# Performance work log

Measured on AMD Instinct MI355X. Metric: run time of the kernel, lower is better.

The kernel has to match this reference:

```python
import jax, jax.numpy as jnp
import numpy as np

B = 8192          # batch
FEAT = 14 * 14 * (16 + 4)  # 3920 features per image
NUM_CLASSES = 10
REPS = 8          # CX+RY repetitions in the filter circuit


def _filter_probs(p):
    """Analytic output distribution of the 4-qubit filter circuit.
    p: (..., 4) pixel angles [p0, p1, p2, p3].
    Circuit: RY(p_i) on qubit i, then 8x [CX(0,1); RY(p0,0)], measure all.
    Qubits 2,3 stay in product state; evolve (q0,q1) as a real 2x2 amplitude
    grid a[q0, q1]. Output index = q0*8 + q1*4 + q2*2 + q3 (Qiskit bitstring
    reversed as in the torch source).
    """
    h = 0.5 * p
    c, s = jnp.cos(h), jnp.sin(h)
    v0 = jnp.stack([c[..., 0], s[..., 0]], axis=-1)
    v1 = jnp.stack([c[..., 1], s[..., 1]], axis=-1)
    a = v0[..., :, None] * v1[..., None, :]        # (..., 2, 2) amplitudes a[q0,q1]
    c0, s0 = c[..., 0], s[..., 0]
    R0 = jnp.stack([jnp.stack([c0, -s0], axis=-1),
                    jnp.stack([s0,  c0], axis=-1)], axis=-2)  # RY(p0) matrix
    for _ in range(REPS):
        # CX(control=q0, target=q1): flip q1 where q0 == 1
        a = jnp.stack([a[..., 0, :], a[..., 1, ::-1]], axis=-2)
        # RY(p0) on q0
        a = jnp.einsum('...ik,...kj->...ij', R0, a)
    P01 = a * a                                    # joint probs over (q0, q1)
    p2 = s[..., 2] ** 2                            # P(q2 = 1)
    p3 = s[..., 3] ** 2                            # P(q3 = 1)
    P2 = jnp.stack([1.0 - p2, p2], axis=-1)
    P3 = jnp.stack([1.0 - p3, p3], axis=-1)
    P = (P01[..., :, :, None, None]
         * P2[..., None, None, :, None]
         * P3[..., None, None, None, :])           # (..., q0, q1, q2, q3)
    return P.reshape(P.shape[:-4] + (16,))


def _sampler_probs(tl, br):
    """2-qubit sampler with all weights = 0: the two CX(0,1) cancel, so the
    state is RY(tl)|0> x RY(br)|0>. Output index = q0*2 + q1."""
    s0 = jnp.sin(0.5 * tl) ** 2   # P(q0 = 1)
    s1 = jnp.sin(0.5 * br) ** 2   # P(q1 = 1)
    return jnp.stack([(1 - s0) * (1 - s1), (1 - s0) * s1,
                      s0 * (1 - s1), s0 * s1], axis=-1)


def setup_inputs() -> dict:
    key = jax.random.key(0)
    k1, k2 = jax.random.split(key)
    x = jax.random.uniform(k1, (B, 1, 28, 28), dtype=jnp.float32)
    fc_w = jax.random.normal(k2, (NUM_CLASSES, FEAT), dtype=jnp.float32) * (FEAT ** -0.5)
    fc_b = jnp.zeros((NUM_CLASSES,), dtype=jnp.float32)
    return {"x": x, "fc_w": fc_w, "fc_b": fc_b}


def reference(x, fc_w, fc_b):
    b = x.shape[0]
    # (b, 14, 14, 2, 2) patches; patch[u, v] = img[2i+u, 2j+v]
    patches = x.reshape(b, 14, 2, 14, 2).transpose(0, 1, 3, 2, 4)
    p = patches.reshape(b, 196, 4)                 # [p0, p1, p2, p3] per patch
    filter_feats = _filter_probs(p).reshape(b, -1)            # (b, 196*16)
    sampler_feats = _sampler_probs(patches[..., 0, 0],
                                   patches[..., 1, 1]).reshape(b, -1)  # (b, 196*4)
    feats = jnp.concatenate([filter_feats, sampler_feats], axis=-1)
    logits = feats @ fc_w.T + fc_b
    return jax.nn.log_softmax(logits, axis=-1)
```

## Files before the change

### kernel.cpp

```cpp
#include <hip/hip_runtime.h>
#include <hip/hip_bf16.h>

typedef float v2f __attribute__((ext_vector_type(2)));
typedef short short8 __attribute__((ext_vector_type(8)));
typedef float f32x4 __attribute__((ext_vector_type(4)));

#define NCLS  10
#define FEATN 3920
#define GIMG  16
#define RSTR  996

__device__ __forceinline__ unsigned packbf(float a, float b) {
    __hip_bfloat162 h = __float22bfloat162_rn(float2{a, b});
    unsigned u; __builtin_memcpy(&u, &h, 4); return u;
}

__global__ void conv_w(const float* __restrict__ fc_w, __hip_bfloat16* __restrict__ ws) {
    const int id = blockIdx.x * 256 + threadIdx.x;
    const int kb = id >> 9;
    const int r  = id & 511;
    const int l  = r >> 3;
    const int j  = r & 7;
    const int n  = l & 15;
    const int k  = kb * 32 + ((l >> 4) << 3) + j;
    const float w = (n < NCLS && k < FEATN) ? fc_w[n * FEATN + k] : 0.f;
    ws[id] = __float2bfloat16(w);
}

__device__ __forceinline__ void do_filter(const float* __restrict__ base, int p, int q,
                                          int dw, unsigned* __restrict__ lds) {
    const int pi = p / 14, pj = p - pi * 14;
    const int offT = pi * 56 + pj * 2;
    const float* iA = base + (size_t)(2 * q) * 784;
    const float* iB = iA + 784;
    const float2 tA = *reinterpret_cast<const float2*>(iA + offT);
    const float2 bA = *reinterpret_cast<const float2*>(iA + offT + 28);
    const float2 tB = *reinterpret_cast<const float2*>(iB + offT);
    const float2 bB = *reinterpret_cast<const float2*>(iB + offT + 28);

    float sA0,cA0,sA1,cA1,sA2,cA2,sA3,cA3;
    float sB0,cB0,sB1,cB1,sB2,cB2,sB3,cB3;
    __sincosf(0.5f * tA.x, &sA0, &cA0); __sincosf(0.5f * tA.y, &sA1, &cA1);
    __sincosf(0.5f * bA.x, &sA2, &cA2); __sincosf(0.5f * bA.y, &sA3, &cA3);
    __sincosf(0.5f * tB.x, &sB0, &cB0); __sincosf(0.5f * tB.y, &sB1, &cB1);
    __sincosf(0.5f * bB.x, &sB2, &cB2); __sincosf(0.5f * bB.y, &sB3, &cB3);

    const v2f c0 = {cA0, cB0}, s0 = {sA0, sB0};
    const v2f c1 = {cA1, cB1}, s1 = {sA1, sB1};
    v2f a00 = c0 * c1, a01 = c0 * s1, a10 = s0 * c1, a11 = s0 * s1;
    #pragma unroll
    for (int r = 0; r < 8; ++r) {
        const v2f b10 = a11, b11 = a10;
        const v2f n00 = c0 * a00 - s0 * b10;
        const v2f n01 = c0 * a01 - s0 * b11;
        const v2f n10 = s0 * a00 + c0 * b10;
        const v2f n11 = s0 * a01 + c0 * b11;
        a00 = n00; a01 = n01; a10 = n10; a11 = n11;
    }
    v2f P2[4];
    P2[0] = a00 * a00; P2[1] = a01 * a01; P2[2] = a10 * a10; P2[3] = a11 * a11;
    const v2f t2c = {cA2*cA2, cB2*cB2}, t2s = {sA2*sA2, sB2*sB2};
    const v2f t3c = {cA3*cA3, cB3*cB3}, t3s = {sA3*sA3, sB3*sB3};
    v2f T[4];
    T[0] = t2c * t3c; T[1] = t2c * t3s; T[2] = t2s * t3c; T[3] = t2s * t3s;

    unsigned dA[8], dB[8];
    #pragma unroll
    for (int m = 0; m < 4; ++m) {
        const v2f f0 = P2[m] * T[0], f1 = P2[m] * T[1];
        const v2f f2 = P2[m] * T[2], f3 = P2[m] * T[3];
        dA[2*m]   = packbf(f0.x, f1.x); dA[2*m+1] = packbf(f2.x, f3.x);
        dB[2*m]   = packbf(f0.y, f1.y); dB[2*m+1] = packbf(f2.y, f3.y);
    }
    unsigned* rowA = lds + (2 * q) * RSTR + dw;
    unsigned* rowB = rowA + RSTR;
    *reinterpret_cast<uint4*>(rowA)     = uint4{dA[0], dA[1], dA[2], dA[3]};
    *reinterpret_cast<uint4*>(rowA + 4) = uint4{dA[4], dA[5], dA[6], dA[7]};
    *reinterpret_cast<uint4*>(rowB)     = uint4{dB[0], dB[1], dB[2], dB[3]};
    *reinterpret_cast<uint4*>(rowB + 4) = uint4{dB[4], dB[5], dB[6], dB[7]};
}

__device__ __forceinline__ void do_sampler(const float* __restrict__ base, int p, int q,
                                           unsigned* __restrict__ lds) {
    const int pi = p / 14, pj = p - pi * 14;
    const int offT = pi * 56 + pj * 2;
    const float* iA = base + (size_t)(2 * q) * 784;
    const float* iB = iA + 784;
    const float p0A = iA[offT],  p3A = iA[offT + 29];
    const float p0B = iB[offT],  p3B = iB[offT + 29];
    const float sA = __sinf(0.5f * p0A), tA = __sinf(0.5f * p3A);
    const float sB = __sinf(0.5f * p0B), tB = __sinf(0.5f * p3B);
    const float saA = sA*sA, sbA = tA*tA, naA = 1.f - saA, nbA = 1.f - sbA;
    const float saB = sB*sB, sbB = tB*tB, naB = 1.f - saB, nbB = 1.f - sbB;
    const int dw = 576 + 2 * p;
    *reinterpret_cast<uint2*>(lds + (2*q)   * RSTR + dw) =
        uint2{packbf(naA*nbA, naA*sbA), packbf(saA*nbA, saA*sbA)};
    *reinterpret_cast<uint2*>(lds + (2*q+1) * RSTR + dw) =
        uint2{packbf(naB*nbB, naB*sbB), packbf(saB*nbB, saB*sbB)};
}

__global__ __launch_bounds__(256, 2)
void quanv_mfma(const float* __restrict__ x,
                const short* __restrict__ wsb,
                const float* __restrict__ fc_b,
                float* __restrict__ out) {
    __shared__ __align__(16) unsigned lds[GIMG * RSTR];
    const int tid  = threadIdx.x;
    const int img0 = blockIdx.x * GIMG;
    const float* base = x + (size_t)img0 * 784;
    const int lane = tid & 63;
    const int wave = tid >> 6;
    const int am   = lane & 15;
    const int ach  = lane >> 4;
    const unsigned aoff = am * RSTR + ach * 4;

    f32x4 acc = {0.f, 0.f, 0.f, 0.f};

    #pragma unroll
    for (int i = 0; i < 4; ++i) {
        const int tau = tid + (i << 8);
        if (tau < 992) do_filter(base, tau >> 3, tau & 7, (tau >> 3) << 3, lds);
    }
    __syncthreads();
    for (int kb = wave; kb < 62; kb += 4) {
        const short8 a = *reinterpret_cast<const short8*>(lds + aoff + kb * 16);
        const short8 b = *reinterpret_cast<const short8*>(wsb + (size_t)kb * 512 + lane * 8);
        acc = __builtin_amdgcn_mfma_f32_16x16x32_bf16(a, b, acc, 0, 0, 0);
    }
    __syncthreads();

    #pragma unroll
    for (int i = 0; i < 3; ++i) {
        const int tau = tid + (i << 8);
        if (tau < 576) {
            const int p = 124 + (tau >> 3);
            do_filter(base, p, tau & 7, (p - 124) << 3, lds);
        }
    }
    #pragma unroll
    for (int i = 0; i < 7; ++i) {
        const int ka = tid + (i << 8);
        if (ka < 1568) do_sampler(base, ka >> 3, ka & 7, lds);
    }
    if (tid < GIMG) {
        unsigned* z = lds + tid * RSTR + 968;
        *reinterpret_cast<uint4*>(z)     = uint4{0, 0, 0, 0};
        *reinterpret_cast<uint4*>(z + 4) = uint4{0, 0, 0, 0};
    }
    __syncthreads();
    for (int kb = wave; kb < 61; kb += 4) {
        const short8 a = *reinterpret_cast<const short8*>(lds + aoff + kb * 16);
        const short8 b = *reinterpret_cast<const short8*>(wsb + (size_t)(62 + kb) * 512 + lane * 8);
        acc = __builtin_amdgcn_mfma_f32_16x16x32_bf16(a, b, acc, 0, 0, 0);
    }
    __syncthreads();

    float* f = reinterpret_cast<float*>(lds);
    f[wave * 256 +   0 + lane] = acc[0];
    f[wave * 256 +  64 + lane] = acc[1];
    f[wave * 256 + 128 + lane] = acc[2];
    f[wave * 256 + 192 + lane] = acc[3];
    __syncthreads();
    if (tid < GIMG * NCLS) {
        const int g = tid / NCLS, c = tid - g * NCLS;
        const int li = ((g >> 2) << 4) + c;
        const int ri = (g & 3) << 6;
        float v = f[ri + li] + f[256 + ri + li] + f[512 + ri + li] + f[768 + ri + li];
        f[1024 + tid] = v + fc_b[c];
    }
    __syncthreads();
    if (tid < GIMG * NCLS) {
        const int g = tid / NCLS, c = tid - g * NCLS;
        const float* lg = f + 1024 + g * NCLS;
        float m = -1e30f;
        #pragma unroll
        for (int k = 0; k < NCLS; ++k) m = fmaxf(m, lg[k]);
        float ss = 0.f;
        #pragma unroll
        for (int k = 0; k < NCLS; ++k) ss += __expf(lg[k] - m);
        out[(size_t)(img0 + g) * NCLS + c] = lg[c] - m - __logf(ss);
    }
}

extern "C" void kernel_launch(void* const* d_in, const int* in_sizes, int n_in,
                              void* d_out, int out_size, void* d_ws, size_t ws_size,
                              hipStream_t stream) {
    const float* x    = (const float*)d_in[0];
    const float* fc_w = (const float*)d_in[1];
    const float* fc_b = (const float*)d_in[2];
    float* out = (float*)d_out;

    conv_w<<<246, 256, 0, stream>>>(fc_w, (__hip_bfloat16*)d_ws);

    const int B = in_sizes[0] / 784;
    const int grid = B / GIMG;
    quanv_mfma<<<grid, 256, 0, stream>>>(x, (const short*)d_ws, fc_b, out);
}
```

Measured before the change: 88.34 us.

## Fuse sampler into filter pass, chunk patches into four stages, halve images per block

Reorders the weight matrix so that each chunk of 48 (or 52) patches has its filter and sampler features contiguous. Each thread computes sampler probabilities from the sincos values it already has, so the separate sampler pass and its extra global loads go away. All pixels are preloaded into registers up front, and the GEMM runs in four chunked stages with a smaller LDS buffer. Images per block drop from 16 to 8 to raise occupancy. Half of the MFMA M dimension now holds duplicate rows, and each stage adds extra barriers.

```diff
diff --git a/kernel.cpp b/kernel.cpp
--- a/kernel.cpp
+++ b/kernel.cpp
@@ -7,8 +7,8 @@
 
 #define NCLS  10
 #define FEATN 3920
-#define GIMG  16
-#define RSTR  996
+#define GIMG  8
+#define RSTR  532
 
 __device__ __forceinline__ unsigned packbf(float a, float b) {
     __hip_bfloat162 h = __float22bfloat162_rn(float2{a, b});
@@ -17,143 +17,138 @@
 
 __global__ void conv_w(const float* __restrict__ fc_w, __hip_bfloat16* __restrict__ ws) {
     const int id = blockIdx.x * 256 + threadIdx.x;
-    const int kb = id >> 9;
-    const int r  = id & 511;
-    const int l  = r >> 3;
-    const int j  = r & 7;
+    if (id >= 123 * 512) return;
+    const int kb = id >> 9, r = id & 511, l = r >> 3, j0 = r & 7;
     const int n  = l & 15;
-    const int k  = kb * 32 + ((l >> 4) << 3) + j;
-    const float w = (n < NCLS && k < FEATN) ? fc_w[n * FEATN + k] : 0.f;
+    const int kk = kb * 32 + ((l >> 4) << 3) + j0;
+    float w = 0.f;
+    if (n < NCLS) {
+        const int t    = (kk < 2880) ? kk / 960 : 3;
+        const int base = 960 * t;
+        const int P0   = 48 * t;
+        const int np   = (t == 3) ? 52 : 48;
+        const int u    = kk - base;
+        int korig = -1;
+        if (u < np * 16) {
+            korig = 16 * (P0 + (u >> 4)) + (u & 15);
+        } else {
+            const int v = u - np * 16;
+            if (v < np * 4) korig = 3136 + 4 * (P0 + (v >> 2)) + (v & 3);
+        }
+        if (korig >= 0) w = fc_w[n * FEATN + korig];
+    }
     ws[id] = __float2bfloat16(w);
 }
 
-__device__ __forceinline__ void do_filter(const float* __restrict__ base, int p, int q,
-                                          int dw, unsigned* __restrict__ lds) {
-    const int pi = p / 14, pj = p - pi * 14;
-    const int offT = pi * 56 + pj * 2;
-    const float* iA = base + (size_t)(2 * q) * 784;
-    const float* iB = iA + 784;
-    const float2 tA = *reinterpret_cast<const float2*>(iA + offT);
-    const float2 bA = *reinterpret_cast<const float2*>(iA + offT + 28);
-    const float2 tB = *reinterpret_cast<const float2*>(iB + offT);
-    const float2 bB = *reinterpret_cast<const float2*>(iB + offT + 28);
-
-    float sA0,cA0,sA1,cA1,sA2,cA2,sA3,cA3;
-    float sB0,cB0,sB1,cB1,sB2,cB2,sB3,cB3;
-    __sincosf(0.5f * tA.x, &sA0, &cA0); __sincosf(0.5f * tA.y, &sA1, &cA1);
-    __sincosf(0.5f * bA.x, &sA2, &cA2); __sincosf(0.5f * bA.y, &sA3, &cA3);
-    __sincosf(0.5f * tB.x, &sB0, &cB0); __sincosf(0.5f * tB.y, &sB1, &cB1);
-    __sincosf(0.5f * bB.x, &sB2, &cB2); __sincosf(0.5f * bB.y, &sB3, &cB3);
-
-    const v2f c0 = {cA0, cB0}, s0 = {sA0, sB0};
-    const v2f c1 = {cA1, cB1}, s1 = {sA1, sB1};
-    v2f a00 = c0 * c1, a01 = c0 * s1, a10 = s0 * c1, a11 = s0 * s1;
-    #pragma unroll
-    for (int r = 0; r < 8; ++r) {
-        const v2f b10 = a11, b11 = a10;
-        const v2f n00 = c0 * a00 - s0 * b10;
-        const v2f n01 = c0 * a01 - s0 * b11;
-        const v2f n10 = s0 * a00 + c0 * b10;
-        const v2f n11 = s0 * a01 + c0 * b11;
-        a00 = n00; a01 = n01; a10 = n10; a11 = n11;
-    }
-    v2f P2[4];
-    P2[0] = a00 * a00; P2[1] = a01 * a01; P2[2] = a10 * a10; P2[3] = a11 * a11;
-    const v2f t2c = {cA2*cA2, cB2*cB2}, t2s = {sA2*sA2, sB2*sB2};
-    const v2f t3c = {cA3*cA3, cB3*cB3}, t3s = {sA3*sA3, sB3*sB3};
-    v2f T[4];
-    T[0] = t2c * t3c; T[1] = t2c * t3s; T[2] = t2s * t3c; T[3] = t2s * t3s;
-
-    unsigned dA[8], dB[8];
-    #pragma unroll
-    for (int m = 0; m < 4; ++m) {
-        const v2f f0 = P2[m] * T[0], f1 = P2[m] * T[1];
-        const v2f f2 = P2[m] * T[2], f3 = P2[m] * T[3];
-        dA[2*m]   = packbf(f0.x, f1.x); dA[2*m+1] = packbf(f2.x, f3.x);
-        dB[2*m]   = packbf(f0.y, f1.y); dB[2*m+1] = packbf(f2.y, f3.y);
-    }
-    unsigned* rowA = lds + (2 * q) * RSTR + dw;
-    unsigned* rowB = rowA + RSTR;
-    *reinterpret_cast<uint4*>(rowA)     = uint4{dA[0], dA[1], dA[2], dA[3]};
-    *reinterpret_cast<uint4*>(rowA + 4) = uint4{dA[4], dA[5], dA[6], dA[7]};
-    *reinterpret_cast<uint4*>(rowB)     = uint4{dB[0], dB[1], dB[2], dB[3]};
-    *reinterpret_cast<uint4*>(rowB + 4) = uint4{dB[4], dB[5], dB[6], dB[7]};
-}
-
-__device__ __forceinline__ void do_sampler(const float* __restrict__ base, int p, int q,
-                                           unsigned* __restrict__ lds) {
-    const int pi = p / 14, pj = p - pi * 14;
-    const int offT = pi * 56 + pj * 2;
-    const float* iA = base + (size_t)(2 * q) * 784;
-    const float* iB = iA + 784;
-    const float p0A = iA[offT],  p3A = iA[offT + 29];
-    const float p0B = iB[offT],  p3B = iB[offT + 29];
-    const float sA = __sinf(0.5f * p0A), tA = __sinf(0.5f * p3A);
-    const float sB = __sinf(0.5f * p0B), tB = __sinf(0.5f * p3B);
-    const float saA = sA*sA, sbA = tA*tA, naA = 1.f - saA, nbA = 1.f - sbA;
-    const float saB = sB*sB, sbB = tB*tB, naB = 1.f - saB, nbB = 1.f - sbB;
-    const int dw = 576 + 2 * p;
-    *reinterpret_cast<uint2*>(lds + (2*q)   * RSTR + dw) =
-        uint2{packbf(naA*nbA, naA*sbA), packbf(saA*nbA, saA*sbA)};
-    *reinterpret_cast<uint2*>(lds + (2*q+1) * RSTR + dw) =
-        uint2{packbf(naB*nbB, naB*sbB), packbf(saB*nbB, saB*sbB)};
-}
-
-__global__ __launch_bounds__(256, 2)
+__global__ __launch_bounds__(256, 4)
 void quanv_mfma(const float* __restrict__ x,
                 const short* __restrict__ wsb,
                 const float* __restrict__ fc_b,
                 float* __restrict__ out) {
     __shared__ __align__(16) unsigned lds[GIMG * RSTR];
     const int tid  = threadIdx.x;
+    const int lane = tid & 63;
+    const int wave = tid >> 6;
     const int img0 = blockIdx.x * GIMG;
     const float* base = x + (size_t)img0 * 784;
-    const int lane = tid & 63;
-    const int wave = tid >> 6;
-    const int am   = lane & 15;
-    const int ach  = lane >> 4;
-    const unsigned aoff = am * RSTR + ach * 4;
+    const int am  = lane & 15;
+    const int ach = lane >> 4;
+    const unsigned aoff = (unsigned)((am & 7) * RSTR + ach * 4);
+
+    float2 pix[4][4];
+    int lpv[4], qv[4];
+    bool act[4];
+    #pragma unroll
+    for (int t = 0; t < 4; ++t) {
+        const int np = (t == 3) ? 52 : 48;
+        const int P0 = 48 * t;
+        const bool a = tid < np * 4;
+        const int tt = a ? tid : 0;
+        const int q  = tt / np;
+        const int lp = tt - q * np;
+        const int p  = P0 + lp;
+        const int pi = p / 14, pj = p - pi * 14;
+        const int off = pi * 56 + pj * 2;
+        const float* iA = base + (size_t)(2 * q) * 784;
+        pix[t][0] = *reinterpret_cast<const float2*>(iA + off);
+        pix[t][1] = *reinterpret_cast<const float2*>(iA + off + 28);
+        pix[t][2] = *reinterpret_cast<const float2*>(iA + 784 + off);
+        pix[t][3] = *reinterpret_cast<const float2*>(iA + 784 + off + 28);
+        lpv[t] = lp; qv[t] = q; act[t] = a;
+    }
 
     f32x4 acc = {0.f, 0.f, 0.f, 0.f};
 
     #pragma unroll
-    for (int i = 0; i < 4; ++i) {
-        const int tau = tid + (i << 8);
-        if (tau < 992) do_filter(base, tau >> 3, tau & 7, (tau >> 3) << 3, lds);
+    for (int t = 0; t < 4; ++t) {
+        const int np  = (t == 3) ? 52 : 48;
+        const int nkb = (t == 3) ? 33 : 30;
+        const int kbb = 30 * t;
+
+        if (act[t]) {
+            const float2 tA = pix[t][0], bA = pix[t][1];
+            const float2 tB = pix[t][2], bB = pix[t][3];
+            float sA0,cA0,sA1,cA1,sA2,cA2,sA3,cA3;
+            float sB0,cB0,sB1,cB1,sB2,cB2,sB3,cB3;
+            __sincosf(0.5f * tA.x, &sA0, &cA0); __sincosf(0.5f * tA.y, &sA1, &cA1);
+            __sincosf(0.5f * bA.x, &sA2, &cA2); __sincosf(0.5f * bA.y, &sA3, &cA3);
+            __sincosf(0.5f * tB.x, &sB0, &cB0); __sincosf(0.5f * tB.y, &sB1, &cB1);
+            __sincosf(0.5f * bB.x, &sB2, &cB2); __sincosf(0.5f * bB.y, &sB3, &cB3);
+
+            const v2f c0 = {cA0, cB0}, s0 = {sA0, sB0};
+            const v2f c1 = {cA1, cB1}, s1 = {sA1, sB1};
+            v2f a00 = c0 * c1, a01 = c0 * s1, a10 = s0 * c1, a11 = s0 * s1;
+            #pragma unroll
+            for (int r = 0; r < 8; ++r) {
+                const v2f b10 = a11, b11 = a10;
+                const v2f n00 = c0 * a00 - s0 * b10;
+                const v2f n01 = c0 * a01 - s0 * b11;
+                const v2f n10 = s0 * a00 + c0 * b10;
+                const v2f n11 = s0 * a01 + c0 * b11;
+                a00 = n00; a01 = n01; a10 = n10; a11 = n11;
+            }
+            v2f P2[4];
+            P2[0] = a00 * a00; P2[1] = a01 * a01; P2[2] = a10 * a10; P2[3] = a11 * a11;
+            const v2f t2c = {cA2*cA2, cB2*cB2}, t2s = {sA2*sA2, sB2*sB2};
+            const v2f t3c = {cA3*cA3, cB3*cB3}, t3s = {sA3*sA3, sB3*sB3};
+            v2f T[4];
+            T[0] = t2c * t3c; T[1] = t2c * t3s; T[2] = t2s * t3c; T[3] = t2s * t3s;
+
+            unsigned dA[8], dB[8];
+            #pragma unroll
+            for (int m = 0; m < 4; ++m) {
+                const v2f f0 = P2[m] * T[0], f1 = P2[m] * T[1];
+                const v2f f2 = P2[m] * T[2], f3 = P2[m] * T[3];
+                dA[2*m]   = packbf(f0.x, f1.x); dA[2*m+1] = packbf(f2.x, f3.x);
+                dB[2*m]   = packbf(f0.y, f1.y); dB[2*m+1] = packbf(f2.y, f3.y);
+            }
+            const v2f sa = s0 * s0, sb = t3s;
+            const v2f na = 1.0f - sa, nb = 1.0f - sb;
+            const v2f e0 = na * nb, e1 = na * sb, e2 = sa * nb, e3 = sa * sb;
+
+            const int lp = lpv[t], q = qv[t];
+            unsigned* rowA = lds + (2 * q) * RSTR;
+            unsigned* rowB = rowA + RSTR;
+            *reinterpret_cast<uint4*>(rowA + lp * 8)     = uint4{dA[0], dA[1], dA[2], dA[3]};
+            *reinterpret_cast<uint4*>(rowA + lp * 8 + 4) = uint4{dA[4], dA[5], dA[6], dA[7]};
+            *reinterpret_cast<uint2*>(rowA + np * 8 + lp * 2) =
+                uint2{packbf(e0.x, e1.x), packbf(e2.x, e3.x)};
+            *reinterpret_cast<uint4*>(rowB + lp * 8)     = uint4{dB[0], dB[1], dB[2], dB[3]};
+            *reinterpret_cast<uint4*>(rowB + lp * 8 + 4) = uint4{dB[4], dB[5], dB[6], dB[7]};
+            *reinterpret_cast<uint2*>(rowB + np * 8 + lp * 2) =
+                uint2{packbf(e0.y, e1.y), packbf(e2.y, e3.y)};
+        }
+        if (t == 3 && tid < 64)
+            lds[(tid >> 3) * RSTR + 520 + (tid & 7)] = 0u;
+        __syncthreads();
+
+        for (int kb = wave; kb < nkb; kb += 4) {
+            const short8 a = *reinterpret_cast<const short8*>(lds + aoff + kb * 16);
+            const short8 b = *reinterpret_cast<const short8*>(wsb + (size_t)(kbb + kb) * 512 + lane * 8);
+            acc = __builtin_amdgcn_mfma_f32_16x16x32_bf16(a, b, acc, 0, 0, 0);
+        }
+        __syncthreads();
     }
-    __syncthreads();
-    for (int kb = wave; kb < 62; kb += 4) {
-        const short8 a = *reinterpret_cast<const short8*>(lds + aoff + kb * 16);
-        const short8 b = *reinterpret_cast<const short8*>(wsb + (size_t)kb * 512 + lane * 8);
-        acc = __builtin_amdgcn_mfma_f32_16x16x32_bf16(a, b, acc, 0, 0, 0);
-    }
-    __syncthreads();
-
-    #pragma unroll
-    for (int i = 0; i < 3; ++i) {
-        const int tau = tid + (i << 8);
-        if (tau < 576) {
-            const int p = 124 + (tau >> 3);
-            do_filter(base, p, tau & 7, (p - 124) << 3, lds);
-        }
-    }
-    #pragma unroll
-    for (int i = 0; i < 7; ++i) {
-        const int ka = tid + (i << 8);
-        if (ka < 1568) do_sampler(base, ka >> 3, ka & 7, lds);
-    }
-    if (tid < GIMG) {
-        unsigned* z = lds + tid * RSTR + 968;
-        *reinterpret_cast<uint4*>(z)     = uint4{0, 0, 0, 0};
-        *reinterpret_cast<uint4*>(z + 4) = uint4{0, 0, 0, 0};
-    }
-    __syncthreads();
-    for (int kb = wave; kb < 61; kb += 4) {
-        const short8 a = *reinterpret_cast<const short8*>(lds + aoff + kb * 16);
-        const short8 b = *reinterpret_cast<const short8*>(wsb + (size_t)(62 + kb) * 512 + lane * 8);
-        acc = __builtin_amdgcn_mfma_f32_16x16x32_bf16(a, b, acc, 0, 0, 0);
-    }
-    __syncthreads();
 
     float* f = reinterpret_cast<float*>(lds);
     f[wave * 256 +   0 + lane] = acc[0];
```

Measured after the change: 85.32 us. -3.4%, faster.
